# Kernel optimization log

Measured on AMD Instinct MI355X. Metric: run time of the kernel, lower is better.

The kernel has to match this reference:

```python
import jax, jax.numpy as jnp
import numpy as np

BETA = 1.0
DEPTH = 10
LEVELS = DEPTH - 1          # decision levels along any root->leaf path
NUM_LEAVES = 2 ** LEVELS    # 512
NUM_INTERNAL = NUM_LEAVES - 1  # 511, heap-ordered: root=0, children 2i+1/2i+2


def _tree_paths():
    """For each leaf, the heap indices of its ancestors and the branch taken (0=left,1=right)."""
    anc = np.zeros((NUM_LEAVES, LEVELS), dtype=np.int32)
    bits = np.zeros((NUM_LEAVES, LEVELS), dtype=np.int32)
    for j in range(NUM_LEAVES):
        node = 0
        for t in range(LEVELS):
            bit = (j >> (LEVELS - 1 - t)) & 1
            anc[j, t] = node
            bits[j, t] = bit
            node = 2 * node + 1 + bit
    return jnp.asarray(anc), jnp.asarray(bits)

_ANC, _BITS = _tree_paths()


def setup_inputs() -> dict:
    key = jax.random.key(0)
    k1, k2, k3, k4 = jax.random.split(key, 4)
    B, F, K = 8192, 4096, 1000
    return {
        "xs": jax.random.normal(k1, (B, F), dtype=jnp.float32),
        "W": jax.random.normal(k2, (NUM_INTERNAL, F), dtype=jnp.float32) * (1.0 / np.sqrt(F)),
        "b": jax.random.normal(k3, (NUM_INTERNAL,), dtype=jnp.float32) * 0.01,
        "leaf_params": jax.random.normal(k4, (NUM_LEAVES, K), dtype=jnp.float32),
    }


def reference(xs, W, b, leaf_params):
    # All node projections as one GEMM: [B, NUM_INTERNAL]
    ps = jax.nn.sigmoid(BETA * (xs @ W.T + b))
    # Gather per-leaf ancestor probs: [B, NUM_LEAVES, LEVELS]
    g = ps[:, _ANC]
    edge = jnp.where(_BITS[None] == 1, g, 1.0 - g)
    leaf_prob = jnp.prod(edge, axis=-1)          # [B, NUM_LEAVES]
    dists = jax.nn.softmax(leaf_params, axis=-1)  # [NUM_LEAVES, K]
    return leaf_prob @ dists                      # [B, K]
```

## Files before the change

### kernel.cpp

```cpp
#include <hip/hip_runtime.h>


typedef __bf16 bf16x8 __attribute__((ext_vector_type(8)));
typedef float f32x4 __attribute__((ext_vector_type(4)));
typedef _Float16 f16x8 __attribute__((ext_vector_type(8)));

#define B_DIM 8192
#define F_DIM 4096
#define NI 511
#define NL 512
#define K_DIM 1000
#define KPAD 1024
#define SPLIT 4
#define KCHUNK 1024

#define W_BLKS  1024
#define SM_BLKS 512

__device__ inline unsigned short f2bf(float f) {
    unsigned int u = __float_as_uint(f);
    return (unsigned short)((u + 0x7FFFu + ((u >> 16) & 1u)) >> 16);
}
__device__ inline unsigned int pk_bf16(float a, float b) {
    return (unsigned int)f2bf(a) | ((unsigned int)f2bf(b) << 16);
}
__device__ inline unsigned int pk2_hu(float a, float b) {
    unsigned int ua = __float_as_uint(a) + 0x8000u;
    unsigned int ub = __float_as_uint(b) + 0x8000u;
    return __builtin_amdgcn_perm(ub, ua, 0x07060302u);
}

typedef __attribute__((address_space(1))) const unsigned int guint;
typedef __attribute__((address_space(3))) unsigned int luint;
__device__ inline void gload16(const unsigned short* g, unsigned short* l) {
    __builtin_amdgcn_global_load_lds((guint*)g, (luint*)l, 16, 0, 0);
}
__device__ inline void gload16f(const float* g, float* l) {
    __builtin_amdgcn_global_load_lds((guint*)g, (luint*)l, 16, 0, 0);
}

__device__ inline bf16x8 ldb(const unsigned short* Lbase, int r, int kb) {
    const int g = (kb >> 3) ^ (r & 7);
    return *(const bf16x8*)&Lbase[r * 64 + g * 8];
}
__device__ inline bf16x8 lda32(const float* Lbase, int r, int kb) {
    const int rs = r & 7;
    const float* rowp = &Lbase[r * 64];
    const f32x4 lo = *(const f32x4*)&rowp[(((kb >> 2)    ) ^ rs) * 4];
    const f32x4 hi = *(const f32x4*)&rowp[(((kb >> 2) + 1) ^ rs) * 4];
    uint4 q;
    q.x = pk2_hu(lo.x, lo.y);
    q.y = pk2_hu(lo.z, lo.w);
    q.z = pk2_hu(hi.x, hi.y);
    q.w = pk2_hu(hi.z, hi.w);
    bf16x8 a;
    __builtin_memcpy(&a, &q, 16);
    return a;
}

__device__ inline float waveMax(float v) {
#pragma unroll
    for (int off = 32; off; off >>= 1) v = fmaxf(v, __shfl_down(v, off, 64));
    return v;
}
__device__ inline float waveSum(float v) {
#pragma unroll
    for (int off = 32; off; off >>= 1) v += __shfl_down(v, off, 64);
    return v;
}

__global__ __launch_bounds__(256) void prep_kernel(
    const float* __restrict__ W, unsigned short* __restrict__ Wb,
    const float* __restrict__ lp, unsigned short* __restrict__ dT)
{
    __shared__ float sred[8];
    const int bid = blockIdx.x;
    const int tid = threadIdx.x;

    if (bid < W_BLKS) {
        const size_t i = ((size_t)bid * 256 + tid) * 8;
        const int row = (int)(i >> 12);
        uint4 h = {0u, 0u, 0u, 0u};
        if (row < NI) {
            const float4 a = *(const float4*)(W + i);
            const float4 b = *(const float4*)(W + i + 4);
            h.x = pk_bf16(a.x, a.y);
            h.y = pk_bf16(a.z, a.w);
            h.z = pk_bf16(b.x, b.y);
            h.w = pk_bf16(b.z, b.w);
        }
        *(uint4*)(Wb + i) = h;
        return;
    }
    const int k = bid - W_BLKS;
    const int lane = tid & 63;
    const int wave = tid >> 6;
    const float* rowp = lp + (size_t)k * K_DIM;

    float vals[4];
    float mx = -3.0e38f;
#pragma unroll
    for (int c = 0; c < 4; ++c) {
        const int n = tid + c * 256;
        vals[c] = (n < K_DIM) ? rowp[n] : -3.0e38f;
        mx = fmaxf(mx, vals[c]);
    }
    mx = waveMax(mx);
    if (lane == 0) sred[wave] = mx;
    __syncthreads();
    const float gmax = fmaxf(fmaxf(sred[0], sred[1]), fmaxf(sred[2], sred[3]));

    float sum = 0.f;
#pragma unroll
    for (int c = 0; c < 4; ++c) {
        const int n = tid + c * 256;
        const float e = (n < K_DIM) ? __expf(vals[c] - gmax) : 0.f;
        vals[c] = e;
        sum += e;
    }
    sum = waveSum(sum);
    if (lane == 0) sred[4 + wave] = sum;
    __syncthreads();
    const float inv = 1.0f / (sred[4] + sred[5] + sred[6] + sred[7]);
#pragma unroll
    for (int c = 0; c < 4; ++c) {
        const int n = tid + c * 256;
        if (n < K_DIM) dT[(size_t)n * NL + k] = f2bf(vals[c] * inv);
    }
}

__global__ __launch_bounds__(256) void gemm1_kernel(
    const float* __restrict__ A, const unsigned short* __restrict__ Bb,
    _Float16* __restrict__ part)
{
    __shared__ __align__(16) float Al[128 * 64];
    __shared__ __align__(16) unsigned short Bl[128 * 64];

    const int id = blockIdx.x;
    const int xcd = id & 7;
    const int jj = (id >> 3) & 15;
    const int mhi = id >> 7;
    const int z = jj >> 2;
    const int nt = jj & 3;
    const int m0 = (mhi * 8 + xcd) * 128;
    const int n0 = nt * 128;
    const int kbeg = z * KCHUNK;

    const int tid = threadIdx.x;
    const int lane = tid & 63;
    const int wave = tid >> 6;
    const int wm = (wave >> 1) * 64;
    const int wn = (wave & 1) * 64;
    const int quad = lane >> 4;
    const int l16 = lane & 15;

    const int dra = lane >> 4;
    const int ca = (((lane & 15) ^ ((wave * 4 + dra) & 7))) * 4;
    const float* gA = A + (size_t)(m0 + wave * 4 + dra) * F_DIM + kbeg + ca;
    float* lA = &Al[wave * 4 * 64];
    const int drb = lane >> 3;
    const int cb = ((lane & 7) ^ drb) * 8;
    const unsigned short* gB = Bb + (size_t)(n0 + wave * 8 + drb) * F_DIM + kbeg + cb;
    unsigned short* lB = &Bl[wave * 8 * 64];

    const f32x4 zero = {0.f, 0.f, 0.f, 0.f};
    f32x4 acc[4][4];
#pragma unroll
    for (int i = 0; i < 4; ++i)
#pragma unroll
        for (int j2 = 0; j2 < 4; ++j2) acc[i][j2] = zero;

    for (int k0 = 0; k0 < KCHUNK; k0 += 64) {
#pragma unroll
        for (int p = 0; p < 8; ++p)
            gload16f(gA + k0 + (size_t)p * 16 * F_DIM, lA + p * 1024);
#pragma unroll
        for (int p = 0; p < 4; ++p)
            gload16(gB + k0 + (size_t)p * 32 * F_DIM, lB + p * 2048);
        __syncthreads();
#pragma unroll
        for (int kk = 0; kk < 64; kk += 32) {
            const int kb = kk + quad * 8;
            bf16x8 av[4], bv[4];
#pragma unroll
            for (int i = 0; i < 4; ++i)
                av[i] = lda32(Al, wm + i * 16 + l16, kb);
#pragma unroll
            for (int j2 = 0; j2 < 4; ++j2)
                bv[j2] = ldb(Bl, wn + j2 * 16 + l16, kb);
#pragma unroll
            for (int i = 0; i < 4; ++i)
#pragma unroll
                for (int j2 = 0; j2 < 4; ++j2)
                    acc[i][j2] = __builtin_amdgcn_mfma_f32_16x16x32_bf16(av[i], bv[j2], acc[i][j2], 0, 0, 0);
        }
        __syncthreads();
    }

    _Float16* dst = part + (size_t)z * ((size_t)B_DIM * NL);
#pragma unroll
    for (int i = 0; i < 4; ++i) {
        const int mbase = m0 + wm + i * 16 + quad * 4;
#pragma unroll
        for (int j2 = 0; j2 < 4; ++j2) {
            const int n = n0 + wn + j2 * 16 + l16;
#pragma unroll
            for (int r = 0; r < 4; ++r)
                dst[(size_t)(mbase + r) * NL + n] = (_Float16)acc[i][j2][r];
        }
    }
}

__global__ __launch_bounds__(256) void reduce_tree_kernel(
    const _Float16* __restrict__ part, const float* __restrict__ bvec,
    unsigned short* __restrict__ leafbf)
{
    __shared__ float bsh[NL];
    __shared__ float prow[4][NL];

    const int tid = threadIdx.x;
    bsh[tid] = (tid < NI) ? bvec[tid] : 0.0f;
    const int t2 = tid + 256;
    bsh[t2] = (t2 < NI) ? bvec[t2] : 0.0f;

    const int wave = tid >> 6;
    const int lane = tid & 63;
    const int row = blockIdx.x * 4 + wave;
    const size_t base = (size_t)row * NL + lane * 8;

    float v[8] = {0.f, 0.f, 0.f, 0.f, 0.f, 0.f, 0.f, 0.f};
#pragma unroll
    for (int s = 0; s < SPLIT; ++s) {
        const f16x8 h = *(const f16x8*)(part + (size_t)s * ((size_t)B_DIM * NL) + base);
#pragma unroll
        for (int e = 0; e < 8; ++e) v[e] += (float)h[e];
    }
    __syncthreads();

#pragma unroll
    for (int i = 0; i < 8; ++i) {
        const float x = v[i] + bsh[lane * 8 + i];
        prow[wave][lane * 8 + i] = 1.0f / (1.0f + __expf(-x));
    }
    __syncthreads();

    const float* pr = prow[wave];
    float pre = 1.0f;
    int pnode = 0;
#pragma unroll
    for (int t = 5; t >= 0; --t) {
        const int bit = (lane >> t) & 1;
        const float p = pr[pnode];
        pre *= bit ? p : (1.0f - p);
        pnode = 2 * pnode + 1 + bit;
    }
    unsigned short outs[8];
#pragma unroll
    for (int jj = 0; jj < 8; ++jj) {
        float prob = pre;
        int node = pnode;
#pragma unroll
        for (int t = 2; t >= 0; --t) {
            const int bit = (jj >> t) & 1;
            const float p = pr[node];
            prob *= bit ? p : (1.0f - p);
            node = 2 * node + 1 + bit;
        }
        outs[jj] = f2bf(prob);
    }
    uint4 r;
    r.x = (unsigned int)outs[0] | ((unsigned int)outs[1] << 16);
    r.y = (unsigned int)outs[2] | ((unsigned int)outs[3] << 16);
    r.z = (unsigned int)outs[4] | ((unsigned int)outs[5] << 16);
    r.w = (unsigned int)outs[6] | ((unsigned int)outs[7] << 16);
    *(uint4*)(leafbf + (size_t)row * NL + lane * 8) = r;
}

__global__ __launch_bounds__(256) void gemm2_kernel(
    const unsigned short* __restrict__ A, const unsigned short* __restrict__ Bm,
    float* __restrict__ out)
{
    __shared__ __align__(16) unsigned short Al[128 * 64];
    __shared__ __align__(16) unsigned short Bl[128 * 64];

    const int id = blockIdx.x;
    const int xcd = id & 7;
    const int j = id >> 3;
    const int nt = j & 7;
    const int mhi = j >> 3;
    const int m0 = (mhi * 8 + xcd) * 128;
    const int n0 = nt * 128;

    const int tid = threadIdx.x;
    const int lane = tid & 63;
    const int wave = tid >> 6;
    const int wm = (wave >> 1) * 64;
    const int wn = (wave & 1) * 64;
    const int quad = lane >> 4;
    const int l16 = lane & 15;

    const int drb = lane >> 3;
    const int cb = ((lane & 7) ^ drb) * 8;
    const unsigned short* gA = A + (size_t)(m0 + wave * 8 + drb) * NL + cb;
    const unsigned short* gB = Bm + (size_t)(n0 + wave * 8 + drb) * NL + cb;
    unsigned short* lA = &Al[wave * 8 * 64];
    unsigned short* lB = &Bl[wave * 8 * 64];

    const f32x4 zero = {0.f, 0.f, 0.f, 0.f};
    f32x4 acc[4][4];
#pragma unroll
    for (int i = 0; i < 4; ++i)
#pragma unroll
        for (int j2 = 0; j2 < 4; ++j2) acc[i][j2] = zero;

    for (int k0 = 0; k0 < NL; k0 += 64) {
#pragma unroll
        for (int p = 0; p < 4; ++p) {
            gload16(gA + k0 + (size_t)p * 32 * NL, lA + p * 2048);
            gload16(gB + k0 + (size_t)p * 32 * NL, lB + p * 2048);
        }
        __syncthreads();
#pragma unroll
        for (int kk = 0; kk < 64; kk += 32) {
            const int kb = kk + quad * 8;
            bf16x8 av[4], bv[4];
#pragma unroll
            for (int i = 0; i < 4; ++i)
                av[i] = ldb(Al, wm + i * 16 + l16, kb);
#pragma unroll
            for (int j2 = 0; j2 < 4; ++j2)
                bv[j2] = ldb(Bl, wn + j2 * 16 + l16, kb);
#pragma unroll
            for (int i = 0; i < 4; ++i)
#pragma unroll
                for (int j2 = 0; j2 < 4; ++j2)
                    acc[i][j2] = __builtin_amdgcn_mfma_f32_16x16x32_bf16(av[i], bv[j2], acc[i][j2], 0, 0, 0);
        }
        __syncthreads();
    }

#pragma unroll
    for (int i = 0; i < 4; ++i) {
        const int mbase = m0 + wm + i * 16 + quad * 4;
#pragma unroll
        for (int j2 = 0; j2 < 4; ++j2) {
            const int n = n0 + wn + j2 * 16 + l16;
            if (n < K_DIM) {
#pragma unroll
                for (int r = 0; r < 4; ++r)
                    out[(size_t)(mbase + r) * K_DIM + n] = acc[i][j2][r];
            }
        }
    }
}

extern "C" void kernel_launch(void* const* d_in, const int* in_sizes, int n_in,
                              void* d_out, int out_size, void* d_ws, size_t ws_size,
                              hipStream_t stream) {
    const float* xs = (const float*)d_in[0];
    const float* W  = (const float*)d_in[1];
    const float* b  = (const float*)d_in[2];
    const float* lp = (const float*)d_in[3];
    float* out = (float*)d_out;

    const size_t partB = (size_t)B_DIM * NL * 2;
    const size_t leafB = (size_t)B_DIM * NL * 2;
    const size_t dTB   = (size_t)KPAD * NL * 2;

    char* ws = (char*)d_ws;
    _Float16* part = (_Float16*)ws;
    unsigned short* leafbf = (unsigned short*)(ws + SPLIT * partB);
    unsigned short* dT = (unsigned short*)(ws + SPLIT * partB + leafB);
    unsigned short* Wb = (unsigned short*)(ws + SPLIT * partB + leafB + dTB);
    (void)ws_size;

    hipLaunchKernelGGL(prep_kernel, dim3(W_BLKS + SM_BLKS), dim3(256), 0, stream,
                       W, Wb, lp, dT);
    hipLaunchKernelGGL(gemm1_kernel, dim3(8 * 8 * 4 * 4), dim3(256), 0, stream,
                       xs, Wb, part);
    hipLaunchKernelGGL(reduce_tree_kernel, dim3(B_DIM / 4), dim3(256), 0, stream,
                       part, b, leafbf);
    hipLaunchKernelGGL(gemm2_kernel, dim3(8 * 8 * 8), dim3(256), 0, stream,
                       leafbf, dT, out);
}
```

Before: 275.3 us.

## Register-prefetch A tile, convert to bf16 before LDS, double-buffer B tile

The fp32 A tile is now loaded into registers one k-step ahead, converted to bf16, and written to a bf16 LDS tile with the same swizzle as B. This replaces the direct fp32 global-to-LDS copy and the per-fragment conversion done at read time. The B tile becomes double-buffered, and the next step's loads are issued before the MFMA loop so memory latency overlaps compute. It uses more registers to hold the prefetched A values and more LDS for the second B buffer, which can reduce occupancy. Correctness depends on the LDS-DMA loads being waited on at the next barrier.

Result: slower. 287.7 us (+4.5%).

```diff
diff --git a/kernel.cpp b/kernel.cpp
--- a/kernel.cpp
+++ b/kernel.cpp
@@ -35,27 +35,10 @@
 __device__ inline void gload16(const unsigned short* g, unsigned short* l) {
     __builtin_amdgcn_global_load_lds((guint*)g, (luint*)l, 16, 0, 0);
 }
-__device__ inline void gload16f(const float* g, float* l) {
-    __builtin_amdgcn_global_load_lds((guint*)g, (luint*)l, 16, 0, 0);
-}
 
 __device__ inline bf16x8 ldb(const unsigned short* Lbase, int r, int kb) {
     const int g = (kb >> 3) ^ (r & 7);
     return *(const bf16x8*)&Lbase[r * 64 + g * 8];
-}
-__device__ inline bf16x8 lda32(const float* Lbase, int r, int kb) {
-    const int rs = r & 7;
-    const float* rowp = &Lbase[r * 64];
-    const f32x4 lo = *(const f32x4*)&rowp[(((kb >> 2)    ) ^ rs) * 4];
-    const f32x4 hi = *(const f32x4*)&rowp[(((kb >> 2) + 1) ^ rs) * 4];
-    uint4 q;
-    q.x = pk2_hu(lo.x, lo.y);
-    q.y = pk2_hu(lo.z, lo.w);
-    q.z = pk2_hu(hi.x, hi.y);
-    q.w = pk2_hu(hi.z, hi.w);
-    bf16x8 a;
-    __builtin_memcpy(&a, &q, 16);
-    return a;
 }
 
 __device__ inline float waveMax(float v) {
@@ -133,8 +116,8 @@
     const float* __restrict__ A, const unsigned short* __restrict__ Bb,
     _Float16* __restrict__ part)
 {
-    __shared__ __align__(16) float Al[128 * 64];
-    __shared__ __align__(16) unsigned short Bl[128 * 64];
+    __shared__ __align__(16) unsigned short Al[128 * 64];
+    __shared__ __align__(16) unsigned short Bl[2][128 * 64];
 
     const int id = blockIdx.x;
     const int xcd = id & 7;
@@ -154,14 +137,14 @@
     const int quad = lane >> 4;
     const int l16 = lane & 15;
 
-    const int dra = lane >> 4;
-    const int ca = (((lane & 15) ^ ((wave * 4 + dra) & 7))) * 4;
-    const float* gA = A + (size_t)(m0 + wave * 4 + dra) * F_DIM + kbeg + ca;
-    float* lA = &Al[wave * 4 * 64];
+    const int rowA = wave * 4 + (lane >> 4);
+    const int q = lane & 15;
+    const float* gA = A + (size_t)(m0 + rowA) * F_DIM + kbeg + q * 4;
+
     const int drb = lane >> 3;
     const int cb = ((lane & 7) ^ drb) * 8;
     const unsigned short* gB = Bb + (size_t)(n0 + wave * 8 + drb) * F_DIM + kbeg + cb;
-    unsigned short* lB = &Bl[wave * 8 * 64];
+    const int lBoff = wave * 8 * 64;
 
     const f32x4 zero = {0.f, 0.f, 0.f, 0.f};
     f32x4 acc[4][4];
@@ -170,24 +153,47 @@
 #pragma unroll
         for (int j2 = 0; j2 < 4; ++j2) acc[i][j2] = zero;
 
-    for (int k0 = 0; k0 < KCHUNK; k0 += 64) {
-#pragma unroll
-        for (int p = 0; p < 8; ++p)
-            gload16f(gA + k0 + (size_t)p * 16 * F_DIM, lA + p * 1024);
-#pragma unroll
-        for (int p = 0; p < 4; ++p)
-            gload16(gB + k0 + (size_t)p * 32 * F_DIM, lB + p * 2048);
+#pragma unroll
+    for (int p = 0; p < 4; ++p)
+        gload16(gB + (size_t)p * 32 * F_DIM, &Bl[0][lBoff + p * 2048]);
+    f32x4 ab[2][8];
+#pragma unroll
+    for (int p = 0; p < 8; ++p)
+        ab[0][p] = *(const f32x4*)(gA + (size_t)p * 16 * F_DIM);
+
+#pragma unroll
+    for (int t = 0; t < 16; ++t) {
+#pragma unroll
+        for (int p = 0; p < 8; ++p) {
+            const int r = rowA + p * 16;
+            uint2 w;
+            w.x = pk2_hu(ab[t & 1][p].x, ab[t & 1][p].y);
+            w.y = pk2_hu(ab[t & 1][p].z, ab[t & 1][p].w);
+            *(uint2*)&Al[r * 64 + (((q >> 1) ^ (r & 7)) * 8) + (q & 1) * 4] = w;
+        }
         __syncthreads();
+
+        if (t < 15) {
+#pragma unroll
+            for (int p = 0; p < 8; ++p)
+                ab[(t + 1) & 1][p] =
+                    *(const f32x4*)(gA + (size_t)(t + 1) * 64 + (size_t)p * 16 * F_DIM);
+#pragma unroll
+            for (int p = 0; p < 4; ++p)
+                gload16(gB + (size_t)(t + 1) * 64 + (size_t)p * 32 * F_DIM,
+                        &Bl[(t + 1) & 1][lBoff + p * 2048]);
+        }
+
 #pragma unroll
         for (int kk = 0; kk < 64; kk += 32) {
             const int kb = kk + quad * 8;
             bf16x8 av[4], bv[4];
 #pragma unroll
             for (int i = 0; i < 4; ++i)
-                av[i] = lda32(Al, wm + i * 16 + l16, kb);
+                av[i] = ldb(Al, wm + i * 16 + l16, kb);
 #pragma unroll
             for (int j2 = 0; j2 < 4; ++j2)
-                bv[j2] = ldb(Bl, wn + j2 * 16 + l16, kb);
+                bv[j2] = ldb(&Bl[t & 1][0], wn + j2 * 16 + l16, kb);
 #pragma unroll
             for (int i = 0; i < 4; ++i)
 #pragma unroll
```
